# Performance work log

Hardware: AMD Instinct MI355X
Metric: run time of the kernel (lower is better)

Reference implementation:

```python
import jax, jax.numpy as jnp
import numpy as np

EPS = 1e-6
DELTA = 1e-6
GAMMA = 1.0


def setup_inputs() -> dict:
    key = jax.random.key(0)
    ks = jax.random.split(key, 6)
    B, N, D, DDIR, DSIM = 2, 384, 256, 128, 64
    sc = lambda d: 1.0 / np.sqrt(d)
    return {
        "t": jax.random.normal(ks[0], (B, N, D), jnp.float32),
        "Qd": jax.random.normal(ks[1], (D, DDIR), jnp.float32) * sc(D),
        "Kd": jax.random.normal(ks[2], (D, DDIR), jnp.float32) * sc(D),
        "Vd": jax.random.normal(ks[3], (DDIR, D), jnp.float32) * sc(DDIR),
        "Qs": jax.random.normal(ks[4], (D, DSIM), jnp.float32) * sc(D),
        "Ks": jax.random.normal(ks[5], (D, DSIM), jnp.float32) * sc(D),
        "a_l": jnp.ones((1,), jnp.float32),
        "b_l": jnp.zeros((1,), jnp.float32),
    }


def reference(t, Qd, Kd, Vd, Qs, Ks, a_l, b_l):
    B, N, D = t.shape
    d_sim = Qs.shape[1]
    # --- similarity: s_ij = <Qs t_i, Ks t_j>/sqrt(d_sim), then symmetrize ---
    q = t @ Qs  # (B,N,d_sim)
    k = t @ Ks
    s = jnp.einsum('bnd,bmd->bnm', q, k) / jnp.sqrt(jnp.float32(d_sim))
    s = 0.5 * (s + s.transpose(0, 2, 1))
    # --- global z-score over off-diagonal entries (biased var) ---
    eye = jnp.eye(N, dtype=bool)[None]  # (1,N,N)
    cnt = jnp.float32(N * (N - 1))
    mu = jnp.where(eye, 0.0, s).sum((1, 2), keepdims=True) / cnt  # (B,1,1)
    var = jnp.where(eye, 0.0, (s - mu) ** 2).sum((1, 2), keepdims=True) / cnt
    s_hat = (s - mu) / jnp.sqrt(var + EPS)
    tilde_s = a_l.reshape(-1, 1, 1) * s_hat + b_l.reshape(-1, 1, 1)
    # --- gates / mass / inertia / apportioned step ---
    A = jax.nn.sigmoid(tilde_s)                                  # (B,N,N)
    m = 1.0 / (jnp.exp(GAMMA * tilde_s).sum(axis=2) + EPS)       # (B,N)
    w = A * m[:, None, :]                                        # w_ij = m_j A_ij
    alpha = A * (w / (w.sum(axis=2, keepdims=True) + DELTA))     # (B,N,N)
    # --- antisymmetric Hadamard direction gate ---
    qd = t @ Qd  # (B,N,d_dir)
    kd = t @ Kd
    had = qd[:, :, None, :] * kd[:, None, :, :]                  # (B,N,N,d_dir)
    kappa = jnp.einsum('bijr,rd->bijd', had, Vd)                 # (B,N,N,D)
    gate = jax.nn.sigmoid(kappa - kappa.transpose(0, 2, 1, 3))
    Dpair = gate * (t[:, :, None, :] - t[:, None, :, :])         # D_ij = gate*(t_i - t_j)
    # --- exclude self pairs, aggregate update ---
    off = ~eye  # (1,N,N)
    alpha = jnp.where(off, alpha, 0.0)
    Dpair = jnp.where(off[..., None], Dpair, 0.0)
    t_next = t - jnp.einsum('bnm,bnmd->bnd', alpha, Dpair)
    return t_next
```

## Files before the change

kernel.cpp:

```cpp
#include <hip/hip_runtime.h>

#define Bn 2
#define Nn 384
#define Dn 256
#define Rn 128
#define Sn 64
#define BNn (Bn*Nn)
#define NEG_LOG2E -1.44269504088896f

typedef short short8 __attribute__((ext_vector_type(8)));
typedef float f32x4 __attribute__((ext_vector_type(4)));
typedef unsigned int uint;
typedef unsigned short ushort;

static __device__ __forceinline__ float fast_sigmoid(float x) {
    return __builtin_amdgcn_rcpf(1.0f + __expf(-x));
}
static __device__ __forceinline__ ushort f2bf(float f) {
    uint u = __float_as_uint(f);
    uint r = (u + 0x7fffu + ((u >> 16) & 1u)) >> 16;
    return (ushort)r;
}
static __device__ __forceinline__ float bf2f(ushort u) {
    return __uint_as_float(((uint)u) << 16);
}

__global__ __launch_bounds__(256)
void prep_kernel(const float* __restrict__ t,
                 const float* __restrict__ Qd, const float* __restrict__ Kd,
                 const float* __restrict__ Vd,
                 const float* __restrict__ Qs, const float* __restrict__ Ks,
                 float* __restrict__ q, float* __restrict__ k,
                 ushort* __restrict__ qdb, ushort* __restrict__ kdb,
                 ushort* __restrict__ VdT, float* __restrict__ stats) {
    const int bi = blockIdx.x;
    const int tid = threadIdx.x;
    if (bi >= BNn) {
        const int idx = (bi - BNn) * 256 + tid;
        const int d = idx >> 7, r = idx & 127;
        VdT[idx] = f2bf(NEG_LOG2E * Vd[(size_t)r * Dn + d]);
        if (bi == BNn && tid < 4) stats[tid] = 0.0f;
        return;
    }
    __shared__ float trow[Dn];
    trow[tid] = t[(size_t)bi * Dn + tid];
    __syncthreads();
    {
        const float* W = (tid < 128) ? Qd : Kd;
        ushort* ob = (tid < 128) ? qdb : kdb;
        const int col = tid & 127;
        float a0 = 0.f;
        for (int kk = 0; kk < Dn; kk += 4) {
            float4 tv = *(const float4*)&trow[kk];
            a0 += tv.x * W[(size_t)(kk + 0) * 128 + col]
                + tv.y * W[(size_t)(kk + 1) * 128 + col]
                + tv.z * W[(size_t)(kk + 2) * 128 + col]
                + tv.w * W[(size_t)(kk + 3) * 128 + col];
        }
        ob[(size_t)bi * 128 + col] = f2bf(a0);
    }
    if (tid < 128) {
        const float* W = (tid < 64) ? Qs : Ks;
        float* of = (tid < 64) ? q : k;
        const int col = tid & 63;
        float a0 = 0.f;
        for (int kk = 0; kk < Dn; kk += 4) {
            float4 tv = *(const float4*)&trow[kk];
            a0 += tv.x * W[(size_t)(kk + 0) * 64 + col]
                + tv.y * W[(size_t)(kk + 1) * 64 + col]
                + tv.z * W[(size_t)(kk + 2) * 64 + col]
                + tv.w * W[(size_t)(kk + 3) * 64 + col];
        }
        of[(size_t)bi * 64 + col] = a0;
    }
}

__global__ __launch_bounds__(256)
void ssym_kernel(const float* __restrict__ q, const float* __restrict__ k,
                 float* __restrict__ ssym, float* __restrict__ stats) {
    __shared__ float qi[16][68], ki[16][68], qj[16][68], kj[16][68];
    __shared__ float part[8];
    const int b = blockIdx.z, it = blockIdx.x, jt = blockIdx.y;
    const int tid = threadIdx.x;
    const int r0 = tid >> 6, c = tid & 63;
#pragma unroll
    for (int p = 0; p < 4; ++p) {
        int row = r0 + 4 * p;
        qi[row][c] = q[((size_t)(b * Nn + it * 16 + row)) * Sn + c];
        ki[row][c] = k[((size_t)(b * Nn + it * 16 + row)) * Sn + c];
        qj[row][c] = q[((size_t)(b * Nn + jt * 16 + row)) * Sn + c];
        kj[row][c] = k[((size_t)(b * Nn + jt * 16 + row)) * Sn + c];
    }
    __syncthreads();
    const int ti = tid >> 4, tj = tid & 15;
    float acc = 0.0f;
#pragma unroll
    for (int dd = 0; dd < Sn; dd += 4) {
        float4 a  = *(const float4*)&qi[ti][dd];
        float4 bb = *(const float4*)&kj[tj][dd];
        float4 cc = *(const float4*)&qj[tj][dd];
        float4 d  = *(const float4*)&ki[ti][dd];
        acc += a.x * bb.x + a.y * bb.y + a.z * bb.z + a.w * bb.w
             + cc.x * d.x + cc.y * d.y + cc.z * d.z + cc.w * d.w;
    }
    const float sval = acc * 0.0625f;
    const int gi = it * 16 + ti, gj = jt * 16 + tj;
    ssym[((size_t)(b * Nn + gi)) * Nn + gj] = sval;
    const float v = (gi == gj) ? 0.0f : sval;

    float vs = v, v2 = v * v;
#pragma unroll
    for (int mask = 32; mask > 0; mask >>= 1) {
        vs += __shfl_xor(vs, mask);
        v2 += __shfl_xor(v2, mask);
    }
    const int lane = tid & 63, wave = tid >> 6;
    if (lane == 0) { part[wave] = vs; part[4 + wave] = v2; }
    __syncthreads();
    if (tid == 0) {
        atomicAdd(&stats[b * 2 + 0], part[0] + part[1] + part[2] + part[3]);
        atomicAdd(&stats[b * 2 + 1], part[4] + part[5] + part[6] + part[7]);
    }
}

__global__ __launch_bounds__(256)
void m_kernel(const float* __restrict__ ssym, const float* __restrict__ stats,
              const float* __restrict__ a_l, const float* __restrict__ b_l,
              float* __restrict__ m) {
    __shared__ float part[4];
    const int row = blockIdx.x;
    const int b = row / Nn;
    const float cnt_inv = 1.0f / (float)(Nn * (Nn - 1));
    const float mu = stats[b * 2 + 0] * cnt_inv;
    const float var = stats[b * 2 + 1] * cnt_inv - mu * mu;
    const float isg = rsqrtf(var + 1e-6f);
    const float a = a_l[0], bbias = b_l[0];
    const int tid = threadIdx.x;
    float sum = __expf(a * (ssym[(size_t)row * Nn + tid] - mu) * isg + bbias);
    if (tid < 128)
        sum += __expf(a * (ssym[(size_t)row * Nn + 256 + tid] - mu) * isg + bbias);
#pragma unroll
    for (int mask = 32; mask > 0; mask >>= 1) sum += __shfl_xor(sum, mask);
    if ((tid & 63) == 0) part[tid >> 6] = sum;
    __syncthreads();
    if (tid == 0) m[row] = 1.0f / (part[0] + part[1] + part[2] + part[3] + 1e-6f);
}

__global__ __launch_bounds__(256, 3)
void pair_kernel(const float* __restrict__ t, const float* __restrict__ ssym,
                 const float* __restrict__ mptr, const float* __restrict__ stats,
                 const float* __restrict__ a_l, const float* __restrict__ b_l,
                 const ushort* __restrict__ qdb, const ushort* __restrict__ kdb,
                 const ushort* __restrict__ VdT, float* __restrict__ out) {
    __shared__ ushort qs_lds[2][4096];
    __shared__ ushort ks_lds[2][4096];
    __shared__ float alpha_s[Nn];
    __shared__ float part[4];

    const int blk = blockIdx.x;
    const int bi = blk >> 1;
    const int dh = blk & 1;
    const int b = bi / Nn;
    const int i = bi - b * Nn;
    const int tid = threadIdx.x;
    const int wave = tid >> 6, lane = tid & 63;
    const int ln = lane & 15, quad = lane >> 4;
    const int wd0 = dh * 128 + wave * 32;

    {
        const float cnt_inv = 1.0f / (float)(Nn * (Nn - 1));
        const float mu = stats[b * 2 + 0] * cnt_inv;
        const float var = stats[b * 2 + 1] * cnt_inv - mu * mu;
        const float isg = rsqrtf(var + 1e-6f);
        const float a = a_l[0], bbias = b_l[0];
        float A0, am0, A1 = 0.f, am1 = 0.f;
        {
            float s0 = ssym[(size_t)bi * Nn + tid];
            A0 = fast_sigmoid(a * (s0 - mu) * isg + bbias);
            am0 = A0 * mptr[b * Nn + tid];
        }
        if (tid < 128) {
            float s1 = ssym[(size_t)bi * Nn + 256 + tid];
            A1 = fast_sigmoid(a * (s1 - mu) * isg + bbias);
            am1 = A1 * mptr[b * Nn + 256 + tid];
        }
        float sum = am0 + am1;
#pragma unroll
        for (int mask = 32; mask > 0; mask >>= 1) sum += __shfl_xor(sum, mask);
        if (lane == 0) part[wave] = sum;
        __syncthreads();
        const float inv = 1.0f / (part[0] + part[1] + part[2] + part[3] + 1e-6f);
        alpha_s[tid] = (tid == i) ? 0.f : A0 * am0 * inv;
        if (tid < 128)
            alpha_s[256 + tid] = ((256 + tid) == i) ? 0.f : A1 * am1 * inv;
    }

    short8 uf[2][4], wf[2][4];
    {
        const size_t qrow = (size_t)bi * Rn;
#pragma unroll
        for (int ks = 0; ks < 4; ++ks) {
            short8 qv = *(const short8*)&qdb[qrow + ks * 32 + quad * 8];
            short8 kv = *(const short8*)&kdb[qrow + ks * 32 + quad * 8];
#pragma unroll
            for (int dt = 0; dt < 2; ++dt) {
                short8 vv = *(const short8*)&VdT[(size_t)(wd0 + dt * 16 + ln) * Rn + ks * 32 + quad * 8];
                short8 uu, ww;
#pragma unroll
                for (int e = 0; e < 8; ++e) {
                    float vf_ = bf2f((ushort)vv[e]);
                    uu[e] = (short)f2bf(vf_ * bf2f((ushort)qv[e]));
                    ww[e] = (short)f2bf(vf_ * bf2f((ushort)kv[e]));
                }
                uf[dt][ks] = uu;
                wf[dt][ks] = ww;
            }
        }
    }

    float4 tiv[2];
    tiv[0] = *(const float4*)&t[(size_t)bi * Dn + wd0 + quad * 4];
    tiv[1] = *(const float4*)&t[(size_t)bi * Dn + wd0 + 16 + quad * 4];
    float4 outac[2];
    outac[0] = make_float4(0.f, 0.f, 0.f, 0.f);
    outac[1] = make_float4(0.f, 0.f, 0.f, 0.f);

    const ushort* qsrc = qdb + (size_t)b * Nn * Rn;
    const ushort* ksrc = kdb + (size_t)b * Nn * Rn;
    const float* tbase_ = t + (size_t)b * Nn * Dn + wd0 + quad * 4;

    const int jr = tid >> 4;
    const int ch = tid & 15;
    const int wb = (ch >> 2) * 1024 + (ch & 3) * 256 + ((jr ^ (ch & 7)) * 16);

    uint4 sq0, sq1, sk0, sk1;

    {
        const ushort* q0 = qsrc + (size_t)jr * Rn + ch * 8;
        const ushort* k0 = ksrc + (size_t)jr * Rn + ch * 8;
        sq0 = *(const uint4*)q0;  sq1 = *(const uint4*)(q0 + 16 * Rn);
        sk0 = *(const uint4*)k0;  sk1 = *(const uint4*)(k0 + 16 * Rn);
        *(uint4*)((char*)&qs_lds[0][0] + wb)        = sq0;
        *(uint4*)((char*)&qs_lds[0][0] + wb + 4096) = sq1;
        *(uint4*)((char*)&ks_lds[0][0] + wb)        = sk0;
        *(uint4*)((char*)&ks_lds[0][0] + wb + 4096) = sk1;
    }
    __syncthreads();

    const int lane_off = ((ln ^ quad) * 16) + quad * 256;

    int cur = 0;
#pragma unroll 1
    for (int tt = 0; tt < Nn / 32; ++tt) {
        const int tn = (tt + 1 < Nn / 32) ? tt + 1 : 0;
        {
            const ushort* q0 = qsrc + (size_t)(tn * 32 + jr) * Rn + ch * 8;
            const ushort* k0 = ksrc + (size_t)(tn * 32 + jr) * Rn + ch * 8;
            sq0 = *(const uint4*)q0;  sq1 = *(const uint4*)(q0 + 16 * Rn);
            sk0 = *(const uint4*)k0;  sk1 = *(const uint4*)(k0 + 16 * Rn);
        }

        const char* qbuf = (const char*)&qs_lds[cur][0];
        const char* kbuf = (const char*)&ks_lds[cur][0];

#pragma unroll
        for (int s = 0; s < 2; ++s) {
            const int jj = tt * 2 + s;
            const int j = jj * 16 + ln;
            const float* tjp = &tbase_[(size_t)j * Dn];
            float4 tj0 = *(const float4*)tjp;
            float4 tj1 = *(const float4*)(tjp + 16);

            f32x4 accU0 = {0.f, 0.f, 0.f, 0.f}, accW0 = {0.f, 0.f, 0.f, 0.f};
            f32x4 accU1 = {0.f, 0.f, 0.f, 0.f}, accW1 = {0.f, 0.f, 0.f, 0.f};
#pragma unroll
            for (int ks = 0; ks < 4; ++ks) {
                const int off = s * 4096 + ks * 1024 + (lane_off ^ ((ks & 1) << 6));
                short8 bk = *(const short8*)(kbuf + off);
                short8 bq = *(const short8*)(qbuf + off);
                accU0 = __builtin_amdgcn_mfma_f32_16x16x32_bf16(uf[0][ks], bk, accU0, 0, 0, 0);
                accU1 = __builtin_amdgcn_mfma_f32_16x16x32_bf16(uf[1][ks], bk, accU1, 0, 0, 0);
                accW0 = __builtin_amdgcn_mfma_f32_16x16x32_bf16(wf[0][ks], bq, accW0, 0, 0, 0);
                accW1 = __builtin_amdgcn_mfma_f32_16x16x32_bf16(wf[1][ks], bq, accW1, 0, 0, 0);
            }
            const float al = alpha_s[j];
            {
                float e0 = accU0[0] - accW0[0];
                float e1 = accU0[1] - accW0[1];
                float e2 = accU0[2] - accW0[2];
                float e3 = accU0[3] - accW0[3];
                float g0 = __builtin_amdgcn_rcpf(1.0f + __builtin_amdgcn_exp2f(e0));
                float g1 = __builtin_amdgcn_rcpf(1.0f + __builtin_amdgcn_exp2f(e1));
                float g2 = __builtin_amdgcn_rcpf(1.0f + __builtin_amdgcn_exp2f(e2));
                float g3 = __builtin_amdgcn_rcpf(1.0f + __builtin_amdgcn_exp2f(e3));
                outac[0].x += al * g0 * (tiv[0].x - tj0.x);
                outac[0].y += al * g1 * (tiv[0].y - tj0.y);
                outac[0].z += al * g2 * (tiv[0].z - tj0.z);
                outac[0].w += al * g3 * (tiv[0].w - tj0.w);
            }
            {
                float e0 = accU1[0] - accW1[0];
                float e1 = accU1[1] - accW1[1];
                float e2 = accU1[2] - accW1[2];
                float e3 = accU1[3] - accW1[3];
                float g0 = __builtin_amdgcn_rcpf(1.0f + __builtin_amdgcn_exp2f(e0));
                float g1 = __builtin_amdgcn_rcpf(1.0f + __builtin_amdgcn_exp2f(e1));
                float g2 = __builtin_amdgcn_rcpf(1.0f + __builtin_amdgcn_exp2f(e2));
                float g3 = __builtin_amdgcn_rcpf(1.0f + __builtin_amdgcn_exp2f(e3));
                outac[1].x += al * g0 * (tiv[1].x - tj1.x);
                outac[1].y += al * g1 * (tiv[1].y - tj1.y);
                outac[1].z += al * g2 * (tiv[1].z - tj1.z);
                outac[1].w += al * g3 * (tiv[1].w - tj1.w);
            }
        }

        {
            char* qd_ = (char*)&qs_lds[cur ^ 1][0];
            char* kd_ = (char*)&ks_lds[cur ^ 1][0];
            *(uint4*)(qd_ + wb)        = sq0;
            *(uint4*)(qd_ + wb + 4096) = sq1;
            *(uint4*)(kd_ + wb)        = sk0;
            *(uint4*)(kd_ + wb + 4096) = sk1;
        }
        __syncthreads();
        cur ^= 1;
    }

#pragma unroll
    for (int dt = 0; dt < 2; ++dt) {
        float4 v = outac[dt];
#pragma unroll
        for (int mask = 1; mask < 16; mask <<= 1) {
            v.x += __shfl_xor(v.x, mask);
            v.y += __shfl_xor(v.y, mask);
            v.z += __shfl_xor(v.z, mask);
            v.w += __shfl_xor(v.w, mask);
        }
        if (ln == 0) {
            float4 o;
            o.x = tiv[dt].x - v.x;
            o.y = tiv[dt].y - v.y;
            o.z = tiv[dt].z - v.z;
            o.w = tiv[dt].w - v.w;
            *(float4*)&out[(size_t)bi * Dn + wd0 + dt * 16 + quad * 4] = o;
        }
    }
}

extern "C" void kernel_launch(void* const* d_in, const int* in_sizes, int n_in,
                              void* d_out, int out_size, void* d_ws, size_t ws_size,
                              hipStream_t stream) {
    const float* t   = (const float*)d_in[0];
    const float* Qd  = (const float*)d_in[1];
    const float* Kd  = (const float*)d_in[2];
    const float* Vd  = (const float*)d_in[3];
    const float* Qs  = (const float*)d_in[4];
    const float* Ks  = (const float*)d_in[5];
    const float* a_l = (const float*)d_in[6];
    const float* b_l = (const float*)d_in[7];
    float* out = (float*)d_out;
    float* ws  = (float*)d_ws;

    float* q     = ws;
    float* k     = q + BNn * Sn;
    float* ssym  = k + BNn * Sn;
    float* m     = ssym + (size_t)BNn * Nn;
    float* stats = m + BNn;
    ushort* qdb  = (ushort*)(stats + 8);
    ushort* kdb  = qdb + (size_t)BNn * Rn;
    ushort* VdT  = kdb + (size_t)BNn * Rn;

    hipLaunchKernelGGL(prep_kernel, dim3(BNn + 128), dim3(256), 0, stream,
                       t, Qd, Kd, Vd, Qs, Ks, q, k, qdb, kdb, VdT, stats);
    hipLaunchKernelGGL(ssym_kernel, dim3(Nn / 16, Nn / 16, Bn), dim3(256), 0, stream,
                       q, k, ssym, stats);
    hipLaunchKernelGGL(m_kernel, dim3(BNn), dim3(256), 0, stream, ssym, stats, a_l, b_l, m);
    hipLaunchKernelGGL(pair_kernel, dim3(BNn * 2), dim3(256), 0, stream,
                       t, ssym, m, stats, a_l, b_l, qdb, kdb, VdT, out);
}
```

Before: 187.9 us.

## Fold antisymmetric gate subtraction into MFMA accumulation and use padded LDS layout

```diff
diff --git a/kernel.cpp b/kernel.cpp
--- a/kernel.cpp
+++ b/kernel.cpp
@@ -146,14 +146,14 @@
     if (tid == 0) m[row] = 1.0f / (part[0] + part[1] + part[2] + part[3] + 1e-6f);
 }
 
-__global__ __launch_bounds__(256, 3)
+__global__ __launch_bounds__(256)
 void pair_kernel(const float* __restrict__ t, const float* __restrict__ ssym,
                  const float* __restrict__ mptr, const float* __restrict__ stats,
                  const float* __restrict__ a_l, const float* __restrict__ b_l,
                  const ushort* __restrict__ qdb, const ushort* __restrict__ kdb,
                  const ushort* __restrict__ VdT, float* __restrict__ out) {
-    __shared__ ushort qs_lds[2][4096];
-    __shared__ ushort ks_lds[2][4096];
+    __shared__ ushort qs_lds[2][32][136];
+    __shared__ ushort ks_lds[2][32][136];
     __shared__ float alpha_s[Nn];
     __shared__ float part[4];
 
@@ -210,7 +210,7 @@
                 for (int e = 0; e < 8; ++e) {
                     float vf_ = bf2f((ushort)vv[e]);
                     uu[e] = (short)f2bf(vf_ * bf2f((ushort)qv[e]));
-                    ww[e] = (short)f2bf(vf_ * bf2f((ushort)kv[e]));
+                    ww[e] = (short)f2bf(-vf_ * bf2f((ushort)kv[e]));
                 }
                 uf[dt][ks] = uu;
                 wf[dt][ks] = ww;
@@ -231,7 +231,6 @@
 
     const int jr = tid >> 4;
     const int ch = tid & 15;
-    const int wb = (ch >> 2) * 1024 + (ch & 3) * 256 + ((jr ^ (ch & 7)) * 16);
 
     uint4 sq0, sq1, sk0, sk1;
 
@@ -240,14 +239,12 @@
         const ushort* k0 = ksrc + (size_t)jr * Rn + ch * 8;
         sq0 = *(const uint4*)q0;  sq1 = *(const uint4*)(q0 + 16 * Rn);
         sk0 = *(const uint4*)k0;  sk1 = *(const uint4*)(k0 + 16 * Rn);
-        *(uint4*)((char*)&qs_lds[0][0] + wb)        = sq0;
-        *(uint4*)((char*)&qs_lds[0][0] + wb + 4096) = sq1;
-        *(uint4*)((char*)&ks_lds[0][0] + wb)        = sk0;
-        *(uint4*)((char*)&ks_lds[0][0] + wb + 4096) = sk1;
-    }
-    __syncthreads();
-
-    const int lane_off = ((ln ^ quad) * 16) + quad * 256;
+        *(uint4*)&qs_lds[0][jr][ch * 8]      = sq0;
+        *(uint4*)&qs_lds[0][jr + 16][ch * 8] = sq1;
+        *(uint4*)&ks_lds[0][jr][ch * 8]      = sk0;
+        *(uint4*)&ks_lds[0][jr + 16][ch * 8] = sk1;
+    }
+    __syncthreads();
 
     int cur = 0;
 #pragma unroll 1
@@ -260,53 +257,42 @@
             sk0 = *(const uint4*)k0;  sk1 = *(const uint4*)(k0 + 16 * Rn);
         }
 
-        const char* qbuf = (const char*)&qs_lds[cur][0];
-        const char* kbuf = (const char*)&ks_lds[cur][0];
-
 #pragma unroll
         for (int s = 0; s < 2; ++s) {
             const int jj = tt * 2 + s;
             const int j = jj * 16 + ln;
+            const int row = s * 16 + ln;
             const float* tjp = &tbase_[(size_t)j * Dn];
             float4 tj0 = *(const float4*)tjp;
             float4 tj1 = *(const float4*)(tjp + 16);
 
-            f32x4 accU0 = {0.f, 0.f, 0.f, 0.f}, accW0 = {0.f, 0.f, 0.f, 0.f};
-            f32x4 accU1 = {0.f, 0.f, 0.f, 0.f}, accW1 = {0.f, 0.f, 0.f, 0.f};
+            f32x4 acc0 = {0.f, 0.f, 0.f, 0.f};
+            f32x4 acc1 = {0.f, 0.f, 0.f, 0.f};
 #pragma unroll
             for (int ks = 0; ks < 4; ++ks) {
-                const int off = s * 4096 + ks * 1024 + (lane_off ^ ((ks & 1) << 6));
-                short8 bk = *(const short8*)(kbuf + off);
-                short8 bq = *(const short8*)(qbuf + off);
-                accU0 = __builtin_amdgcn_mfma_f32_16x16x32_bf16(uf[0][ks], bk, accU0, 0, 0, 0);
-                accU1 = __builtin_amdgcn_mfma_f32_16x16x32_bf16(uf[1][ks], bk, accU1, 0, 0, 0);
-                accW0 = __builtin_amdgcn_mfma_f32_16x16x32_bf16(wf[0][ks], bq, accW0, 0, 0, 0);
-                accW1 = __builtin_amdgcn_mfma_f32_16x16x32_bf16(wf[1][ks], bq, accW1, 0, 0, 0);
+                short8 bk = *(const short8*)&ks_lds[cur][row][ks * 32 + quad * 8];
+                short8 bq = *(const short8*)&qs_lds[cur][row][ks * 32 + quad * 8];
+                acc0 = __builtin_amdgcn_mfma_f32_16x16x32_bf16(uf[0][ks], bk, acc0, 0, 0, 0);
+                acc1 = __builtin_amdgcn_mfma_f32_16x16x32_bf16(uf[1][ks], bk, acc1, 0, 0, 0);
+                acc0 = __builtin_amdgcn_mfma_f32_16x16x32_bf16(wf[0][ks], bq, acc0, 0, 0, 0);
+                acc1 = __builtin_amdgcn_mfma_f32_16x16x32_bf16(wf[1][ks], bq, acc1, 0, 0, 0);
             }
             const float al = alpha_s[j];
             {
-                float e0 = accU0[0] - accW0[0];
-                float e1 = accU0[1] - accW0[1];
-                float e2 = accU0[2] - accW0[2];
-                float e3 = accU0[3] - accW0[3];
-                float g0 = __builtin_amdgcn_rcpf(1.0f + __builtin_amdgcn_exp2f(e0));
-                float g1 = __builtin_amdgcn_rcpf(1.0f + __builtin_amdgcn_exp2f(e1));
-                float g2 = __builtin_amdgcn_rcpf(1.0f + __builtin_amdgcn_exp2f(e2));
-                float g3 = __builtin_amdgcn_rcpf(1.0f + __builtin_amdgcn_exp2f(e3));
+                float g0 = __builtin_amdgcn_rcpf(1.0f + __builtin_amdgcn_exp2f(acc0[0]));
+                float g1 = __builtin_amdgcn_rcpf(1.0f + __builtin_amdgcn_exp2f(acc0[1]));
+                float g2 = __builtin_amdgcn_rcpf(1.0f + __builtin_amdgcn_exp2f(acc0[2]));
+                float g3 = __builtin_amdgcn_rcpf(1.0f + __builtin_amdgcn_exp2f(acc0[3]));
                 outac[0].x += al * g0 * (tiv[0].x - tj0.x);
                 outac[0].y += al * g1 * (tiv[0].y - tj0.y);
                 outac[0].z += al * g2 * (tiv[0].z - tj0.z);
                 outac[0].w += al * g3 * (tiv[0].w - tj0.w);
             }
             {
-                float e0 = accU1[0] - accW1[0];
-                float e1 = accU1[1] - accW1[1];
-                float e2 = accU1[2] - accW1[2];
-                float e3 = accU1[3] - accW1[3];
-                float g0 = __builtin_amdgcn_rcpf(1.0f + __builtin_amdgcn_exp2f(e0));
-                float g1 = __builtin_amdgcn_rcpf(1.0f + __builtin_amdgcn_exp2f(e1));
-                float g2 = __builtin_amdgcn_rcpf(1.0f + __builtin_amdgcn_exp2f(e2));
-                float g3 = __builtin_amdgcn_rcpf(1.0f + __builtin_amdgcn_exp2f(e3));
+                float g0 = __builtin_amdgcn_rcpf(1.0f + __builtin_amdgcn_exp2f(acc1[0]));
+                float g1 = __builtin_amdgcn_rcpf(1.0f + __builtin_amdgcn_exp2f(acc1[1]));
+                float g2 = __builtin_amdgcn_rcpf(1.0f + __builtin_amdgcn_exp2f(acc1[2]));
+                float g3 = __builtin_amdgcn_rcpf(1.0f + __builtin_amdgcn_exp2f(acc1[3]));
                 outac[1].x += al * g0 * (tiv[1].x - tj1.x);
                 outac[1].y += al * g1 * (tiv[1].y - tj1.y);
                 outac[1].z += al * g2 * (tiv[1].z - tj1.z);
@@ -315,12 +301,10 @@
         }
 
         {
-            char* qd_ = (char*)&qs_lds[cur ^ 1][0];
-            char* kd_ = (char*)&ks_lds[cur ^ 1][0];
-            *(uint4*)(qd_ + wb)        = sq0;
-            *(uint4*)(qd_ + wb + 4096) = sq1;
-            *(uint4*)(kd_ + wb)        = sk0;
-            *(uint4*)(kd_ + wb + 4096) = sk1;
+            *(uint4*)&qs_lds[cur ^ 1][jr][ch * 8]      = sq0;
+            *(uint4*)&qs_lds[cur ^ 1][jr + 16][ch * 8] = sq1;
+            *(uint4*)&ks_lds[cur ^ 1][jr][ch * 8]      = sk0;
+            *(uint4*)&ks_lds[cur ^ 1][jr + 16][ch * 8] = sk1;
         }
         __syncthreads();
         cur ^= 1;
```

New measurement: 192.6 us. 1.02x slower.
